# Performance work log

Measured on AMD Instinct MI355X. Metric: run time of the kernel, lower is better.

The kernel has to match this reference:

```python
import jax, jax.numpy as jnp
import numpy as np

B, L, D, H, DFF, V, NL = 8, 512, 1024, 16, 4096, 32000, 6
DH = D // H
EPS = 1e-5


def _layer_norm(x):
    # fresh nn.LayerNorm(d_model) each call: gamma=1, beta=0
    mu = jnp.mean(x, axis=-1, keepdims=True)
    var = jnp.var(x, axis=-1, keepdims=True)
    return (x - mu) / jnp.sqrt(var + EPS)


def _positional_encoding(seq_len, d_model, dtype):
    position = jnp.arange(seq_len, dtype=jnp.float32)[:, None]
    div_term = 1.0 / jnp.power(10000.0, jnp.arange(0, d_model, 2, dtype=jnp.float32) / d_model)
    pe = jnp.zeros((seq_len, d_model), dtype=jnp.float32)
    pe = pe.at[:, 0::2].set(jnp.sin(position * div_term))
    pe = pe.at[:, 1::2].set(jnp.cos(position * div_term))
    return pe.astype(dtype)  # [L, D]


def setup_inputs() -> dict:
    key = jax.random.key(0)
    ks = jax.random.split(key, 16)
    s = 0.02
    inp = {
        "sequence": jax.random.randint(ks[0], (B, L), 0, V),
        "segment_label": jax.random.randint(ks[1], (B, L), 0, 3),
        "tok_emb": jax.random.normal(ks[2], (V, D), jnp.float32) * s,
        "seg_emb": jax.random.normal(ks[3], (3, D), jnp.float32) * s,
        "Wq": jax.random.normal(ks[4], (NL, D, D), jnp.float32) * s,
        "bq": jnp.zeros((NL, D), jnp.float32),
        "Wk": jax.random.normal(ks[5], (NL, D, D), jnp.float32) * s,
        "bk": jnp.zeros((NL, D), jnp.float32),
        "Wv": jax.random.normal(ks[6], (NL, D, D), jnp.float32) * s,
        "bv": jnp.zeros((NL, D), jnp.float32),
        "Wo": jax.random.normal(ks[7], (NL, D, D), jnp.float32) * s,
        "bo": jnp.zeros((NL, D), jnp.float32),
        "W1": jax.random.normal(ks[8], (NL, D, DFF), jnp.float32) * s,
        "b1": jnp.zeros((NL, DFF), jnp.float32),
        "W2": jax.random.normal(ks[9], (NL, DFF, D), jnp.float32) * s,
        "b2": jnp.zeros((NL, D), jnp.float32),
    }
    return inp


def reference(sequence, segment_label, tok_emb, seg_emb, Wq, bq, Wk, bk, Wv, bv, Wo, bo, W1, b1, W2, b2):
    n_layers = Wq.shape[0]
    batch, seq_len = sequence.shape
    d_model = tok_emb.shape[1]
    n_heads = H
    dh = d_model // n_heads

    # pad mask: True where key token == 0; broadcast over heads and query positions
    pad = (sequence == 0)  # [B, Lk]
    mask = pad[:, None, None, :]  # [B, 1, 1, Lk]

    pe = _positional_encoding(seq_len, d_model, tok_emb.dtype)
    x = tok_emb[sequence] + pe[None, :, :] + seg_emb[segment_label]  # [B, L, D]

    for i in range(n_layers):
        residual = x
        # NOTE: original code uses a raw reshape [B, L, H*dh] -> [B, H, L, dh]
        # (no transpose); we replicate that exact math.
        q = (x @ Wq[i] + bq[i]).reshape(batch, n_heads, seq_len, dh)
        k = (x @ Wk[i] + bk[i]).reshape(batch, n_heads, seq_len, dh)
        v = (x @ Wv[i] + bv[i]).reshape(batch, n_heads, seq_len, dh)
        scores = jnp.einsum("bhqd,bhkd->bhqk", q, k) / jnp.sqrt(jnp.asarray(dh, x.dtype))
        scores = jnp.where(mask, jnp.asarray(-1e9, x.dtype), scores)
        attn = jax.nn.softmax(scores, axis=-1)
        context = jnp.einsum("bhqk,bhkd->bhqd", attn, v).reshape(batch, seq_len, n_heads * dh)
        out = context @ Wo[i] + bo[i]
        x = _layer_norm(out + residual)

        residual = x
        h = jax.nn.gelu(x @ W1[i] + b1[i], approximate=False)
        out = h @ W2[i] + b2[i]
        x = _layer_norm(residual + out)

    return x
```

## Files before the change

### kernel.cpp

```cpp
#include <hip/hip_runtime.h>
#include <cstdint>
#include <cstddef>

typedef unsigned short u16;
typedef __attribute__((ext_vector_type(8))) short short8;
typedef __attribute__((ext_vector_type(4))) float f32x4;

#define DEV __device__ __forceinline__

DEV float bf2f(u16 u) {
    union { float f; uint32_t i; } c; c.i = ((uint32_t)u) << 16; return c.f;
}
DEV u16 f2bf(float f) {
    union { float f; uint32_t i; } c; c.f = f;
    uint32_t r = c.i + 0x7FFF + ((c.i >> 16) & 1);
    return (u16)(r >> 16);
}

DEV void gload16(const void* g, void* l) {
    __builtin_amdgcn_global_load_lds(
        (const __attribute__((address_space(1))) void*)g,
        (__attribute__((address_space(3))) void*)l, 16, 0, 0);
}

template<int N> DEV void waitv() {
    if constexpr (N == 0)      asm volatile("s_waitcnt vmcnt(0)" ::: "memory");
    else if constexpr (N == 4) asm volatile("s_waitcnt vmcnt(4)" ::: "memory");
    else if constexpr (N == 8) asm volatile("s_waitcnt vmcnt(8)" ::: "memory");
    else                       asm volatile("s_waitcnt vmcnt(0)" ::: "memory");
}

template<int EPI>
__global__ __launch_bounds__(512)
void gemm256_blk(const u16* __restrict__ Ablk, const u16* __restrict__ Bblk,
                 void* __restrict__ C, const float* __restrict__ bias,
                 int K, int Mtot, int Ntot)
{
    constexpr int THREADS = 512;
    constexpr int BM = 256, BN = 256, BK = 32;
    constexpr int MR = 8, NR = 4;
    __shared__ __align__(16) u16 As[3 * BM * BK];
    __shared__ __align__(16) u16 Bs[3 * BN * BK];

    const int tid = threadIdx.x, lane = tid & 63, wid = tid >> 6;
    const int wr = wid >> 2, wc = wid & 3;
    const int lr = lane & 15, lk = lane >> 4;
    const int m0 = blockIdx.x * BM, n0 = blockIdx.y * BN;
    const long planeA = (long)Mtot * 64, planeB = (long)Ntot * 64;

    f32x4 acc[MR][NR] = {};

    auto stageA = [&](int buf, int k0) {
        const long base = (long)(k0 >> 6) * planeA + (k0 & 32);
#pragma unroll
        for (int i = 0; i < 2; ++i) {
            int ch = i * THREADS + tid;
            int rp = ch >> 3, s = ch & 7, d = s ^ (rp & 7);
            const u16* g = Ablk + base + (long)(m0 + ((rp << 1) | (d & 1))) * 64 + ((d >> 1) << 3);
            gload16(g, (char*)As + (size_t)buf * (BM * BK * 2) + ch * 16);
        }
    };
    auto stageB = [&](int buf, int k0) {
        const long base = (long)(k0 >> 6) * planeB + (k0 & 32);
#pragma unroll
        for (int i = 0; i < 2; ++i) {
            int ch = i * THREADS + tid;
            int rp = ch >> 3, s = ch & 7, d = s ^ (rp & 7);
            const u16* g = Bblk + base + (long)(n0 + ((rp << 1) | (d & 1))) * 64 + ((d >> 1) << 3);
            gload16(g, (char*)Bs + (size_t)buf * (BN * BK * 2) + ch * 16);
        }
    };
    auto lds_off = [&](int row) -> int {
        int rp = row >> 1;
        int s  = ((lk << 1) | (row & 1)) ^ (rp & 7);
        return rp * 64 + s * 8;
    };

    const int nt = K >> 5;

    stageA(0, 0); stageB(0, 0);
    if (nt > 1) { stageA(1, BK); stageB(1, BK); }
    if (nt > 1) waitv<4>(); else waitv<0>();
    __builtin_amdgcn_s_barrier();

    for (int k = 0; k < nt; ++k) {
        const int cur = k % 3;
        const int nxt = (k + 2) % 3;
        const u16* Ac = As + (size_t)cur * (BM * BK);
        const u16* Bc = Bs + (size_t)cur * (BN * BK);
        short8 af[MR], bf[NR];

#pragma unroll
        for (int n = 0; n < NR; ++n)
            bf[n] = *(const short8*)(Bc + lds_off(wc * 64 + n * 16 + lr));
#pragma unroll
        for (int m = 0; m < 4; ++m)
            af[m] = *(const short8*)(Ac + lds_off(wr * 128 + m * 16 + lr));
        if (k + 2 < nt) stageA(nxt, (k + 2) * BK);
        asm volatile("s_waitcnt lgkmcnt(0)" ::: "memory");
        __builtin_amdgcn_s_setprio(1);
#pragma unroll
        for (int m = 0; m < 4; ++m)
#pragma unroll
            for (int n = 0; n < NR; ++n)
                acc[m][n] = __builtin_amdgcn_mfma_f32_16x16x32_bf16(af[m], bf[n], acc[m][n], 0, 0, 0);
        __builtin_amdgcn_s_setprio(0);

#pragma unroll
        for (int m = 4; m < 8; ++m)
            af[m] = *(const short8*)(Ac + lds_off(wr * 128 + m * 16 + lr));
        if (k + 2 < nt) stageB(nxt, (k + 2) * BK);
        asm volatile("s_waitcnt lgkmcnt(0)" ::: "memory");
        __builtin_amdgcn_s_setprio(1);
#pragma unroll
        for (int m = 4; m < 8; ++m)
#pragma unroll
            for (int n = 0; n < NR; ++n)
                acc[m][n] = __builtin_amdgcn_mfma_f32_16x16x32_bf16(af[m], bf[n], acc[m][n], 0, 0, 0);
        __builtin_amdgcn_s_setprio(0);

        if (k + 1 < nt) {
            if (k + 2 < nt) waitv<4>(); else waitv<0>();
            __builtin_amdgcn_s_barrier();
        }
    }

#pragma unroll
    for (int m = 0; m < MR; ++m) {
        const int rowb = m0 + wr * 128 + m * 16 + (lane >> 4) * 4;
#pragma unroll
        for (int n = 0; n < NR; ++n) {
            const int col = n0 + wc * 64 + n * 16 + lr;
            const float bv = bias[col];
#pragma unroll
            for (int j = 0; j < 4; ++j) {
                float v = acc[m][n][j];
                if (EPI == 6) {
                    float t = v + bv;
                    ((u16*)C)[(long)(col >> 6) * 262144L + (long)(rowb + j) * 64 + (col & 63)]
                        = f2bf(0.5f * t * (1.0f + erff(t * 0.70710678118654752f)));
                } else {
                    const long qidx = (long)(col >> 10) * 4194304L
                                    + (long)(rowb + j) * 1024 + (col & 1023);
                    ((u16*)C)[qidx] = f2bf(v + bv);
                }
            }
        }
    }
}

__global__ __launch_bounds__(512)
void gemm_k64(const u16* __restrict__ Ablk, const u16* __restrict__ Bblk,
              float* __restrict__ C, const float* __restrict__ bias,
              const float* __restrict__ resid, int K, int Mtot, int Ntot)
{
    constexpr int THREADS = 512;
    constexpr int BM = 128, BN = 128;
    constexpr int MR = 4, NR = 2;
    __shared__ __align__(16) u16 As[3 * BM * 64];
    __shared__ __align__(16) u16 Bs[3 * BN * 64];

    const int tid = threadIdx.x, lane = tid & 63, wid = tid >> 6;
    const int wr = wid >> 2, wc = wid & 3;
    const int lr = lane & 15, lk = lane >> 4;
    const int m0 = blockIdx.x * BM, n0 = blockIdx.y * BN;
    const long planeA = (long)Mtot * 64, planeB = (long)Ntot * 64;

    f32x4 acc[MR][NR] = {};

    auto stageA = [&](int buf, int k0) {
#pragma unroll
        for (int i = 0; i < 2; ++i) {
            int ch = i * THREADS + tid;
            int row = ch >> 3, s = ch & 7, d = s ^ (row & 7);
            const u16* g = Ablk + (long)(k0 >> 6) * planeA + (long)(m0 + row) * 64 + d * 8;
            gload16(g, (char*)As + (size_t)buf * (BM * 128) + ch * 16);
        }
    };
    auto stageB = [&](int buf, int k0) {
#pragma unroll
        for (int i = 0; i < 2; ++i) {
            int ch = i * THREADS + tid;
            int row = ch >> 3, s = ch & 7, d = s ^ (row & 7);
            const u16* g = Bblk + (long)(k0 >> 6) * planeB + (long)(n0 + row) * 64 + d * 8;
            gload16(g, (char*)Bs + (size_t)buf * (BN * 128) + ch * 16);
        }
    };
    auto lds_off = [&](int row, int ks) -> int {
        return row * 64 + ((ks ^ (row & 7)) << 3);
    };

    const int nt = K >> 6;

    stageA(0, 0); stageB(0, 0);
    if (nt > 1) { stageA(1, 64); stageB(1, 64); }
    if (nt > 2) { stageA(2, 128); stageB(2, 128); }
    if (nt > 2)      waitv<8>();
    else if (nt > 1) waitv<4>();
    else             waitv<0>();
    __builtin_amdgcn_s_barrier();

    for (int k = 0; k < nt; ++k) {
        const int cur = k % 3;
        const u16* Ac = As + (size_t)cur * (BM * 64);
        const u16* Bc = Bs + (size_t)cur * (BN * 64);
        short8 af[2][MR], bf[2][NR];
#pragma unroll
        for (int h = 0; h < 2; ++h) {
#pragma unroll
            for (int m = 0; m < MR; ++m)
                af[h][m] = *(const short8*)(Ac + lds_off(wr * 64 + m * 16 + lr, h * 4 + lk));
#pragma unroll
            for (int n = 0; n < NR; ++n)
                bf[h][n] = *(const short8*)(Bc + lds_off(wc * 32 + n * 16 + lr, h * 4 + lk));
        }

        asm volatile("s_waitcnt lgkmcnt(0)" ::: "memory");
        __builtin_amdgcn_s_barrier();

        if (k + 3 < nt) { stageA(cur, (k + 3) * 64); stageB(cur, (k + 3) * 64); }

        __builtin_amdgcn_s_setprio(1);
#pragma unroll
        for (int h = 0; h < 2; ++h)
#pragma unroll
            for (int m = 0; m < MR; ++m)
#pragma unroll
                for (int n = 0; n < NR; ++n)
                    acc[m][n] = __builtin_amdgcn_mfma_f32_16x16x32_bf16(af[h][m], bf[h][n], acc[m][n], 0, 0, 0);
        __builtin_amdgcn_s_setprio(0);

        if (k + 1 < nt) {
            if (k + 4 <= nt)      waitv<8>();
            else if (k + 3 == nt) waitv<4>();
            else                  waitv<0>();
            __builtin_amdgcn_s_barrier();
        }
    }

#pragma unroll
    for (int m = 0; m < MR; ++m) {
        const int rowb = m0 + wr * 64 + m * 16 + (lane >> 4) * 4;
#pragma unroll
        for (int n = 0; n < NR; ++n) {
            const int col = n0 + wc * 32 + n * 16 + lr;
            const float bv = bias[col];
#pragma unroll
            for (int j = 0; j < 4; ++j) {
                const long idx = (long)(rowb + j) * 1024 + col;
                C[idx] = acc[m][n][j] + bv + resid[idx];
            }
        }
    }
}

__global__ __launch_bounds__(512)
void attn_kernel(const u16* __restrict__ Qb, const u16* __restrict__ Kb,
                 const u16* __restrict__ vt, const int* __restrict__ seq,
                 u16* __restrict__ ctxB)
{
    __shared__ __align__(16) u16 Ss[64 * 512];
    const int lin = blockIdx.y * 8 + blockIdx.x;
    const int L   = (lin & 7) * 128 + (lin >> 3);
    const int bh  = L >> 3;
    const int q0  = (L & 7) << 6;
    const int tid = threadIdx.x, lane = tid & 63, wid = tid >> 6;
    const int b  = bh >> 4;
    const u16* Qh = Qb + ((long)bh << 15) + (long)q0 * 64;
    const u16* Kh = Kb + ((long)bh << 15);
    const u16* Vh = vt + ((long)bh << 15);
    const int lr = lane & 15, lk = lane >> 4;

    f32x4 sacc[4][4] = {};
    {
        short8 af[4], bf[4];
#pragma unroll
        for (int s = 0; s < 2; ++s) {
#pragma unroll
            for (int m = 0; m < 4; ++m)
                af[m] = *(const short8*)(Qh + (long)(m * 16 + lr) * 64 + s * 32 + lk * 8);
#pragma unroll
            for (int n = 0; n < 4; ++n)
                bf[n] = *(const short8*)(Kh + (long)(wid * 64 + n * 16 + lr) * 64 + s * 32 + lk * 8);
#pragma unroll
            for (int m = 0; m < 4; ++m)
#pragma unroll
                for (int n = 0; n < 4; ++n)
                    sacc[m][n] = __builtin_amdgcn_mfma_f32_16x16x32_bf16(af[m], bf[n], sacc[m][n], 0, 0, 0);
        }
    }
#pragma unroll
    for (int m = 0; m < 4; ++m) {
#pragma unroll
        for (int n = 0; n < 4; ++n) {
            const int k = wid * 64 + n * 16 + lr;
#pragma unroll
            for (int j = 0; j < 4; ++j) {
                const int q = m * 16 + (lane >> 4) * 4 + j;
                const int col = (((k >> 3) ^ (q & 7)) << 3) | (k & 7);
                Ss[q * 512 + col] = f2bf(sacc[m][n][j] * 0.125f);
            }
        }
    }
    __syncthreads();

    const int* sq = seq + (b << 9) + (lane << 3);
    int msk[8];
#pragma unroll
    for (int i = 0; i < 8; ++i) msk[i] = sq[i];
#pragma unroll
    for (int r = 0; r < 8; ++r) {
        const int q = wid * 8 + r;
        u16* p = Ss + q * 512 + ((lane ^ (q & 7)) << 3);
        short8 raw = *(short8*)p;
        float v[8];
#pragma unroll
        for (int i = 0; i < 8; ++i)
            v[i] = (msk[i] == 0) ? -1e9f : bf2f((u16)raw[i]);
        float mx = v[0];
#pragma unroll
        for (int i = 1; i < 8; ++i) mx = fmaxf(mx, v[i]);
#pragma unroll
        for (int o = 32; o; o >>= 1) mx = fmaxf(mx, __shfl_xor(mx, o));
        float e[8], sum = 0.f;
#pragma unroll
        for (int i = 0; i < 8; ++i) { e[i] = expf(v[i] - mx); sum += e[i]; }
#pragma unroll
        for (int o = 32; o; o >>= 1) sum += __shfl_xor(sum, o);
        float rr = 1.0f / sum;
        short8 o8;
#pragma unroll
        for (int i = 0; i < 8; ++i) o8[i] = (short)f2bf(e[i] * rr);
        *(short8*)p = o8;
    }
    __syncthreads();

    const int wr = wid >> 1, wc2 = wid & 1;
    f32x4 pacc[2] = {};
#pragma unroll
    for (int ks = 0; ks < 16; ++ks) {
        const int qrow = wr * 16 + lr;
        short8 pa = *(const short8*)(Ss + qrow * 512 + (((ks * 4 + lk) ^ (qrow & 7)) << 3));
        short8 vb[2];
#pragma unroll
        for (int n = 0; n < 2; ++n) {
            const int d = wc2 * 32 + n * 16 + lr;
            vb[n] = *(const short8*)(Vh + (long)d * 512 + ks * 32 + lk * 8);
        }
#pragma unroll
        for (int n = 0; n < 2; ++n)
            pacc[n] = __builtin_amdgcn_mfma_f32_16x16x32_bf16(pa, vb[n], pacc[n], 0, 0, 0);
    }
#pragma unroll
    for (int n = 0; n < 2; ++n) {
        const int d = wc2 * 32 + n * 16 + lr;
#pragma unroll
        for (int j = 0; j < 4; ++j) {
            const int q = wr * 16 + (lane >> 4) * 4 + j;
            const long F = ((long)bh << 15) + (long)(q0 + q) * 64 + d;
            const long r = F >> 10;
            const int  c = (int)(F & 1023);
            ctxB[(long)(c >> 6) * 262144L + r * 64 + (c & 63)] = f2bf(pacc[n][j]);
        }
    }
}

__global__ __launch_bounds__(256)
void wconv_blk(const float* __restrict__ src, u16* __restrict__ dst,
               int N, int planeN, int row_off, long src_z, long dst_z)
{
    __shared__ __align__(16) float t[64][65];
    const int z = blockIdx.z;
    const int k0 = blockIdx.x * 64, n0 = blockIdx.y * 64;
    const float* s = src + (long)z * src_z + (long)k0 * N + n0;
    const int tid = threadIdx.x;
#pragma unroll
    for (int i = 0; i < 4; ++i) {
        int ch = (i << 8) + tid;
        int r = ch >> 4, c4 = ch & 15;
        float4 v = *(const float4*)(s + (long)r * N + c4 * 4);
        t[r][c4 * 4 + 0] = v.x; t[r][c4 * 4 + 1] = v.y;
        t[r][c4 * 4 + 2] = v.z; t[r][c4 * 4 + 3] = v.w;
    }
    __syncthreads();
    u16* d = dst + (long)z * dst_z + (long)blockIdx.x * planeN * 64 + (long)(row_off + n0) * 64;
#pragma unroll
    for (int i = 0; i < 4; ++i) {
        int ch = (i << 8) + tid;
        int c = ch >> 4, k4 = ch & 15;
        ushort4 o;
        o.x = f2bf(t[k4 * 4 + 0][c]);
        o.y = f2bf(t[k4 * 4 + 1][c]);
        o.z = f2bf(t[k4 * 4 + 2][c]);
        o.w = f2bf(t[k4 * 4 + 3][c]);
        *(ushort4*)(d + (long)c * 64 + k4 * 4) = o;
    }
}

__global__ __launch_bounds__(256)
void bconcat_kernel(const float* __restrict__ bq, const float* __restrict__ bk,
                    const float* __restrict__ bv, float* __restrict__ out)
{
    int i = blockIdx.x * 256 + threadIdx.x;
    int l = i / 3072, n = i % 3072;
    float v = (n < 1024) ? bq[l * 1024 + n]
            : (n < 2048) ? bk[l * 1024 + n - 1024]
                         : bv[l * 1024 + n - 2048];
    out[i] = v;
}

__global__ __launch_bounds__(256)
void embed_kernel(const int* __restrict__ seq, const int* __restrict__ seg,
                  const float* __restrict__ tok, const float* __restrict__ sege,
                  float* __restrict__ x, u16* __restrict__ xbB)
{
    long i = ((long)blockIdx.x << 8) + threadIdx.x;
    int d2 = (int)(i & 511);
    long bl = i >> 9;
    int l = (int)(bl & 511);
    int t = seq[bl];
    int g = seg[bl];
    float div = powf(10000.f, -(float)(2 * d2) * (1.0f / 1024.f));
    float arg = (float)l * div;
    float sv = sinf(arg), cv = cosf(arg);
    long toff = (long)t * 1024 + 2 * d2;
    long goff = (long)g * 1024 + 2 * d2;
    float x0 = tok[toff]     + sv + sege[goff];
    float x1 = tok[toff + 1] + cv + sege[goff + 1];
    long xo = (bl << 10) + 2 * d2;
    x[xo] = x0; x[xo + 1] = x1;
    const int c = 2 * d2;
    u16* p = xbB + (long)(c >> 6) * 262144L + bl * 64 + (c & 63);
    p[0] = f2bf(x0); p[1] = f2bf(x1);
}

__global__ __launch_bounds__(256)
void vtrans_kernel(const u16* __restrict__ Vb, u16* __restrict__ vt)
{
    __shared__ __align__(16) u16 t[64][72];
    const int bh = blockIdx.y;
    const int l0 = blockIdx.x << 6;
    const u16* src = Vb + ((long)bh << 15) + (long)l0 * 64;
    const int tid = threadIdx.x;
#pragma unroll
    for (int i = 0; i < 2; ++i) {
        int ch = (i << 8) + tid;
        int r = ch >> 3, c8 = ch & 7;
        short8 v = *(const short8*)(src + (long)r * 64 + (c8 << 3));
#pragma unroll
        for (int j = 0; j < 8; ++j) t[r][(c8 << 3) + j] = (u16)v[j];
    }
    __syncthreads();
    u16* d = vt + ((long)bh << 15) + l0;
#pragma unroll
    for (int i = 0; i < 2; ++i) {
        int ch = (i << 8) + tid;
        int dd = ch >> 3, l8 = ch & 7;
        short8 o;
#pragma unroll
        for (int j = 0; j < 8; ++j) o[j] = (short)t[(l8 << 3) + j][dd];
        *(short8*)(d + (long)dd * 512 + (l8 << 3)) = o;
    }
}

__global__ __launch_bounds__(256)
void ln_kernel(const float* __restrict__ in, float* __restrict__ xout, u16* __restrict__ xbB)
{
    const int row = blockIdx.x;
    const int tid = threadIdx.x;
    const float4 v = ((const float4*)(in + (long)row * 1024))[tid];
    float s = v.x + v.y + v.z + v.w;
#pragma unroll
    for (int o = 32; o; o >>= 1) s += __shfl_down(s, o);
    __shared__ float red[8];
    const int wid = tid >> 6, lane = tid & 63;
    if (lane == 0) red[wid] = s;
    __syncthreads();
    const float mean = (red[0] + red[1] + red[2] + red[3]) * (1.0f / 1024.f);
    const float dx = v.x - mean, dy = v.y - mean, dz = v.z - mean, dw = v.w - mean;
    float q = dx * dx + dy * dy + dz * dz + dw * dw;
#pragma unroll
    for (int o = 32; o; o >>= 1) q += __shfl_down(q, o);
    if (lane == 0) red[4 + wid] = q;
    __syncthreads();
    const float var = (red[4] + red[5] + red[6] + red[7]) * (1.0f / 1024.f);
    const float inv = rsqrtf(var + 1e-5f);
    float4 o4;
    o4.x = dx * inv; o4.y = dy * inv; o4.z = dz * inv; o4.w = dw * inv;
    ((float4*)(xout + (long)row * 1024))[tid] = o4;
    ushort4 ob;
    ob.x = f2bf(o4.x); ob.y = f2bf(o4.y); ob.z = f2bf(o4.z); ob.w = f2bf(o4.w);
    *(ushort4*)(xbB + (long)(tid >> 4) * 262144L + (long)row * 64 + (tid & 15) * 4) = ob;
}

extern "C" void kernel_launch(void* const* d_in, const int* in_sizes, int n_in,
                              void* d_out, int out_size, void* d_ws, size_t ws_size,
                              hipStream_t stream)
{
    const int*   seqp = (const int*)d_in[0];
    const int*   segp = (const int*)d_in[1];
    const float* tok  = (const float*)d_in[2];
    const float* sege = (const float*)d_in[3];
    const float* Wq = (const float*)d_in[4];  const float* bq = (const float*)d_in[5];
    const float* Wk = (const float*)d_in[6];  const float* bk = (const float*)d_in[7];
    const float* Wv = (const float*)d_in[8];  const float* bv = (const float*)d_in[9];
    const float* Wo = (const float*)d_in[10]; const float* bo = (const float*)d_in[11];
    const float* W1 = (const float*)d_in[12]; const float* b1 = (const float*)d_in[13];
    const float* W2 = (const float*)d_in[14]; const float* b2 = (const float*)d_in[15];

    char* w = (char*)d_ws;
    auto take = [&](size_t bytes) -> void* {
        void* p = (void*)w; w += (bytes + 255) & ~(size_t)255; return p;
    };
    float* x    = (float*)take(4096UL * 1024 * 4);
    u16*   xbB  = (u16*)  take(4096UL * 1024 * 2);
    float* tmp  = (float*)take(4096UL * 1024 * 4);
    u16*   hbuf = (u16*)  take(4096UL * 4096 * 2);
    u16*   qkv3 = (u16*)  take(3UL * 4096 * 1024 * 2);
    u16*   ctxB = (u16*)  take(4096UL * 1024 * 2);
    u16*   vt   = (u16*)  take(128UL * 64 * 512 * 2);
    u16*   qkvwB= (u16*)  take(6UL * 3072 * 1024 * 2);
    u16*   woB  = (u16*)  take(6UL * 1024 * 1024 * 2);
    u16*   w1B  = (u16*)  take(6UL * 4096 * 1024 * 2);
    u16*   w2B  = (u16*)  take(6UL * 1024 * 4096 * 2);
    float* bqkv = (float*)take(6UL * 3072 * 4);

    u16* Qb = qkv3;
    u16* Kb = qkv3 + 4194304L;
    u16* Vb = qkv3 + 8388608L;

    bconcat_kernel<<<72, 256, 0, stream>>>(bq, bk, bv, bqkv);
    wconv_blk<<<dim3(16, 16, 6), 256, 0, stream>>>(Wq, qkvwB, 1024, 3072, 0,    1048576L, 3145728L);
    wconv_blk<<<dim3(16, 16, 6), 256, 0, stream>>>(Wk, qkvwB, 1024, 3072, 1024, 1048576L, 3145728L);
    wconv_blk<<<dim3(16, 16, 6), 256, 0, stream>>>(Wv, qkvwB, 1024, 3072, 2048, 1048576L, 3145728L);
    wconv_blk<<<dim3(16, 16, 6), 256, 0, stream>>>(Wo, woB,   1024, 1024, 0,    1048576L, 1048576L);
    wconv_blk<<<dim3(16, 64, 6), 256, 0, stream>>>(W1, w1B,   4096, 4096, 0,    4194304L, 4194304L);
    wconv_blk<<<dim3(64, 16, 6), 256, 0, stream>>>(W2, w2B,   1024, 1024, 0,    4194304L, 4194304L);

    embed_kernel<<<8192, 256, 0, stream>>>(seqp, segp, tok, sege, x, xbB);

    for (int l = 0; l < 6; ++l) {
        gemm256_blk<5><<<dim3(16, 12), 512, 0, stream>>>(
            xbB, qkvwB + (long)l * 3145728L, qkv3, bqkv + l * 3072,
            1024, 4096, 3072);

        vtrans_kernel<<<dim3(8, 128), 256, 0, stream>>>(Vb, vt);

        attn_kernel<<<dim3(8, 128), 512, 0, stream>>>(Qb, Kb, vt, seqp, ctxB);

        gemm_k64<<<dim3(32, 8), 512, 0, stream>>>(
            ctxB, woB + (long)l * 1048576L, tmp, bo + l * 1024, x,
            1024, 4096, 1024);

        ln_kernel<<<4096, 256, 0, stream>>>(tmp, x, xbB);

        gemm256_blk<6><<<dim3(16, 16), 512, 0, stream>>>(
            xbB, w1B + (long)l * 4194304L, hbuf, b1 + l * 4096,
            1024, 4096, 4096);

        gemm_k64<<<dim3(32, 8), 512, 0, stream>>>(
            hbuf, w2B + (long)l * 4194304L, tmp, b2 + l * 1024, x,
            4096, 4096, 1024);

        ln_kernel<<<4096, 256, 0, stream>>>(tmp, (l == 5) ? (float*)d_out : x, xbB);
    }
}
```

Before: 1.629 ms.

## Restructure 256x256 GEMM into 8-phase schedule with BK=64 double buffering

Replaces the triple-buffered BK=32 main loop of the large GEMM with a BK=64 double-buffered loop. Each K-tile is split into four LDS-read/MFMA phases with interleaved half-tile global-to-LDS loads and block barriers between phases. The aim is to overlap global loads with matrix-core work more finely and halve the number of main-loop iterations, at the cost of more barriers per iteration and a different buffer-reuse hazard pattern. The LDS layout changes from row-pair swizzling to a per-row XOR swizzle over 64-wide K slices.

```diff
diff --git a/kernel.cpp b/kernel.cpp
--- a/kernel.cpp
+++ b/kernel.cpp
@@ -32,113 +32,154 @@
 
 template<int EPI>
 __global__ __launch_bounds__(512)
-void gemm256_blk(const u16* __restrict__ Ablk, const u16* __restrict__ Bblk,
+void gemm256_8ph(const u16* __restrict__ Ablk, const u16* __restrict__ Bblk,
                  void* __restrict__ C, const float* __restrict__ bias,
                  int K, int Mtot, int Ntot)
 {
     constexpr int THREADS = 512;
-    constexpr int BM = 256, BN = 256, BK = 32;
-    constexpr int MR = 8, NR = 4;
-    __shared__ __align__(16) u16 As[3 * BM * BK];
-    __shared__ __align__(16) u16 Bs[3 * BN * BK];
+    __shared__ __align__(16) u16 As[4 * 8192];
+    __shared__ __align__(16) u16 Bs[4 * 8192];
 
     const int tid = threadIdx.x, lane = tid & 63, wid = tid >> 6;
     const int wr = wid >> 2, wc = wid & 3;
     const int lr = lane & 15, lk = lane >> 4;
-    const int m0 = blockIdx.x * BM, n0 = blockIdx.y * BN;
+    const int m0 = blockIdx.x * 256, n0 = blockIdx.y * 256;
     const long planeA = (long)Mtot * 64, planeB = (long)Ntot * 64;
 
-    f32x4 acc[MR][NR] = {};
-
-    auto stageA = [&](int buf, int k0) {
-        const long base = (long)(k0 >> 6) * planeA + (k0 & 32);
+    f32x4 acc[8][4] = {};
+
+    auto stageA = [&](int t, int h) {
+        u16* dst = As + (size_t)((t & 1) * 2 + h) * 8192;
 #pragma unroll
         for (int i = 0; i < 2; ++i) {
             int ch = i * THREADS + tid;
-            int rp = ch >> 3, s = ch & 7, d = s ^ (rp & 7);
-            const u16* g = Ablk + base + (long)(m0 + ((rp << 1) | (d & 1))) * 64 + ((d >> 1) << 3);
-            gload16(g, (char*)As + (size_t)buf * (BM * BK * 2) + ch * 16);
+            int row = ch >> 3, s = ch & 7, d = s ^ (row & 7);
+            const u16* g = Ablk + (long)t * planeA + (long)(m0 + h * 128 + row) * 64 + d * 8;
+            gload16(g, (char*)dst + ch * 16);
         }
     };
-    auto stageB = [&](int buf, int k0) {
-        const long base = (long)(k0 >> 6) * planeB + (k0 & 32);
+    auto stageB = [&](int t, int h) {
+        u16* dst = Bs + (size_t)((t & 1) * 2 + h) * 8192;
 #pragma unroll
         for (int i = 0; i < 2; ++i) {
             int ch = i * THREADS + tid;
-            int rp = ch >> 3, s = ch & 7, d = s ^ (rp & 7);
-            const u16* g = Bblk + base + (long)(n0 + ((rp << 1) | (d & 1))) * 64 + ((d >> 1) << 3);
-            gload16(g, (char*)Bs + (size_t)buf * (BN * BK * 2) + ch * 16);
+            int row = ch >> 3, s = ch & 7, d = s ^ (row & 7);
+            const u16* g = Bblk + (long)t * planeB + (long)(n0 + h * 128 + row) * 64 + d * 8;
+            gload16(g, (char*)dst + ch * 16);
         }
     };
-    auto lds_off = [&](int row) -> int {
-        int rp = row >> 1;
-        int s  = ((lk << 1) | (row & 1)) ^ (rp & 7);
-        return rp * 64 + s * 8;
+    auto loff = [&](int row, int ks) -> int {
+        return row * 64 + ((ks ^ (row & 7)) << 3);
     };
 
-    const int nt = K >> 5;
-
-    stageA(0, 0); stageB(0, 0);
-    if (nt > 1) { stageA(1, BK); stageB(1, BK); }
-    if (nt > 1) waitv<4>(); else waitv<0>();
+    const int nt = K >> 6;
+
+    stageA(0, 0); stageA(0, 1); stageB(0, 0); stageB(0, 1);
+    stageA(1, 0); stageA(1, 1); stageB(1, 0); stageB(1, 1);
+    waitv<8>();
     __builtin_amdgcn_s_barrier();
 
-    for (int k = 0; k < nt; ++k) {
-        const int cur = k % 3;
-        const int nxt = (k + 2) % 3;
-        const u16* Ac = As + (size_t)cur * (BM * BK);
-        const u16* Bc = Bs + (size_t)cur * (BN * BK);
-        short8 af[MR], bf[NR];
-
-#pragma unroll
-        for (int n = 0; n < NR; ++n)
-            bf[n] = *(const short8*)(Bc + lds_off(wc * 64 + n * 16 + lr));
+    for (int t = 0; t < nt; ++t) {
+        const int p = t & 1;
+        const u16* Ah  = As + (size_t)(p * 2 + wr) * 8192;
+        const u16* Bh  = Bs + (size_t)(p * 2 + (wc >> 1)) * 8192;
+        const int brow = (wc & 1) * 64;
+        short8 af[4][2], bf[4][2];
+
 #pragma unroll
         for (int m = 0; m < 4; ++m)
-            af[m] = *(const short8*)(Ac + lds_off(wr * 128 + m * 16 + lr));
-        if (k + 2 < nt) stageA(nxt, (k + 2) * BK);
+#pragma unroll
+            for (int kh = 0; kh < 2; ++kh)
+                af[m][kh] = *(const short8*)(Ah + loff(m * 16 + lr, kh * 4 + lk));
+#pragma unroll
+        for (int n = 0; n < 2; ++n)
+#pragma unroll
+            for (int kh = 0; kh < 2; ++kh)
+                bf[n][kh] = *(const short8*)(Bh + loff(brow + n * 16 + lr, kh * 4 + lk));
+        if (t >= 1 && t + 1 < nt) stageA(t + 1, 0);
         asm volatile("s_waitcnt lgkmcnt(0)" ::: "memory");
+        __builtin_amdgcn_s_barrier();
         __builtin_amdgcn_s_setprio(1);
 #pragma unroll
+        for (int kh = 0; kh < 2; ++kh)
+#pragma unroll
+            for (int m = 0; m < 4; ++m)
+#pragma unroll
+                for (int n = 0; n < 2; ++n)
+                    acc[m][n] = __builtin_amdgcn_mfma_f32_16x16x32_bf16(af[m][kh], bf[n][kh], acc[m][n], 0, 0, 0);
+        __builtin_amdgcn_s_setprio(0);
+        __builtin_amdgcn_s_barrier();
+
+#pragma unroll
+        for (int n = 2; n < 4; ++n)
+#pragma unroll
+            for (int kh = 0; kh < 2; ++kh)
+                bf[n][kh] = *(const short8*)(Bh + loff(brow + n * 16 + lr, kh * 4 + lk));
+        if (t >= 1 && t + 1 < nt) stageA(t + 1, 1);
+        asm volatile("s_waitcnt lgkmcnt(0)" ::: "memory");
+        __builtin_amdgcn_s_barrier();
+        __builtin_amdgcn_s_setprio(1);
+#pragma unroll
+        for (int kh = 0; kh < 2; ++kh)
+#pragma unroll
+            for (int m = 0; m < 4; ++m)
+#pragma unroll
+                for (int n = 2; n < 4; ++n)
+                    acc[m][n] = __builtin_amdgcn_mfma_f32_16x16x32_bf16(af[m][kh], bf[n][kh], acc[m][n], 0, 0, 0);
+        __builtin_amdgcn_s_setprio(0);
+        __builtin_amdgcn_s_barrier();
+
+#pragma unroll
         for (int m = 0; m < 4; ++m)
 #pragma unroll
-            for (int n = 0; n < NR; ++n)
-                acc[m][n] = __builtin_amdgcn_mfma_f32_16x16x32_bf16(af[m], bf[n], acc[m][n], 0, 0, 0);
+            for (int kh = 0; kh < 2; ++kh)
+                af[m][kh] = *(const short8*)(Ah + loff((m + 4) * 16 + lr, kh * 4 + lk));
+        if (t + 2 < nt) stageB(t + 2, 0);
+        asm volatile("s_waitcnt lgkmcnt(0)" ::: "memory");
+        __builtin_amdgcn_s_barrier();
+        __builtin_amdgcn_s_setprio(1);
+#pragma unroll
+        for (int kh = 0; kh < 2; ++kh)
+#pragma unroll
+            for (int m = 0; m < 4; ++m)
+#pragma unroll
+                for (int n = 2; n < 4; ++n)
+                    acc[m + 4][n] = __builtin_amdgcn_mfma_f32_16x16x32_bf16(af[m][kh], bf[n][kh], acc[m + 4][n], 0, 0, 0);
         __builtin_amdgcn_s_setprio(0);
-
-#pragma unroll
-        for (int m = 4; m < 8; ++m)
-            af[m] = *(const short8*)(Ac + lds_off(wr * 128 + m * 16 + lr));
-        if (k + 2 < nt) stageB(nxt, (k + 2) * BK);
-        asm volatile("s_waitcnt lgkmcnt(0)" ::: "memory");
+        __builtin_amdgcn_s_barrier();
+
+        if (t + 2 < nt) stageB(t + 2, 1);
+        __builtin_amdgcn_s_barrier();
         __builtin_amdgcn_s_setprio(1);
 #pragma unroll
-        for (int m = 4; m < 8; ++m)
-#pragma unroll
-            for (int n = 0; n < NR; ++n)
-                acc[m][n] = __builtin_amdgcn_mfma_f32_16x16x32_bf16(af[m], bf[n], acc[m][n], 0, 0, 0);
+        for (int kh = 0; kh < 2; ++kh)
+#pragma unroll
+            for (int m = 0; m < 4; ++m)
+#pragma unroll
+                for (int n = 0; n < 2; ++n)
+                    acc[m + 4][n] = __builtin_amdgcn_mfma_f32_16x16x32_bf16(af[m][kh], bf[n][kh], acc[m + 4][n], 0, 0, 0);
         __builtin_amdgcn_s_setprio(0);
 
-        if (k + 1 < nt) {
-            if (k + 2 < nt) waitv<4>(); else waitv<0>();
+        if (t + 1 < nt) {
+            if (t + 2 < nt) waitv<4>(); else waitv<0>();
             __builtin_amdgcn_s_barrier();
         }
     }
 
 #pragma unroll
-    for (int m = 0; m < MR; ++m) {
+    for (int m = 0; m < 8; ++m) {
         const int rowb = m0 + wr * 128 + m * 16 + (lane >> 4) * 4;
 #pragma unroll
-        for (int n = 0; n < NR; ++n) {
+        for (int n = 0; n < 4; ++n) {
             const int col = n0 + wc * 64 + n * 16 + lr;
             const float bv = bias[col];
 #pragma unroll
             for (int j = 0; j < 4; ++j) {
                 float v = acc[m][n][j];
                 if (EPI == 6) {
-                    float t = v + bv;
+                    float tt = v + bv;
                     ((u16*)C)[(long)(col >> 6) * 262144L + (long)(rowb + j) * 64 + (col & 63)]
-                        = f2bf(0.5f * t * (1.0f + erff(t * 0.70710678118654752f)));
+                        = f2bf(0.5f * tt * (1.0f + erff(tt * 0.70710678118654752f)));
                 } else {
                     const long qidx = (long)(col >> 10) * 4194304L
                                     + (long)(rowb + j) * 1024 + (col & 1023);
@@ -540,7 +581,7 @@
     embed_kernel<<<8192, 256, 0, stream>>>(seqp, segp, tok, sege, x, xbB);
 
     for (int l = 0; l < 6; ++l) {
-        gemm256_blk<5><<<dim3(16, 12), 512, 0, stream>>>(
+        gemm256_8ph<5><<<dim3(16, 12), 512, 0, stream>>>(
             xbB, qkvwB + (long)l * 3145728L, qkv3, bqkv + l * 3072,
             1024, 4096, 3072);
 
@@ -554,7 +595,7 @@
 
         ln_kernel<<<4096, 256, 0, stream>>>(tmp, x, xbB);
 
-        gemm256_blk<6><<<dim3(16, 16), 512, 0, stream>>>(
+        gemm256_8ph<6><<<dim3(16, 16), 512, 0, stream>>>(
             xbB, w1B + (long)l * 4194304L, hbuf, b1 + l * 4096,
             1024, 4096, 4096);
 
```

Result: no change. 1.629 ms (-0.0%).
